# Kernel tuning notes

Hardware: AMD Instinct MI355X
Metric: run time of the kernel (lower is better)

Reference implementation:

```python
import jax, jax.numpy as jnp
import numpy as np

B = 65536       # batch size
C = 100         # num classes (len(cls_num_list))
ALPHA = 0.01    # soft-label blend weight
TAU = 2.0       # init arg tau
TEMP = 2.0      # distillation temperature
EPS = 1e-9


def _soft_ce(logits, soft_targets):
    # -(soft * log softmax(logits)).sum(1).mean()
    return -(soft_targets * jax.nn.log_softmax(logits, axis=1)).sum(axis=1).mean()


def _inverse_prior(prior):
    idx0 = jnp.argsort(prior)            # ascending sort permutation
    value = prior[idx0]                  # sorted values
    idx1 = jnp.argsort(idx0)             # rank of each element
    idx2 = prior.shape[0] - 1 - idx1     # mirrored rank
    return value[idx2]


def setup_inputs():
    key = jax.random.key(0)
    ks = jax.random.split(key, 8)
    cls_num = np.arange(500, 0, -5).astype(np.float32)  # matches init cls_num_list
    prior = jnp.asarray(cls_num / cls_num.sum(), dtype=jnp.float32)
    return {
        "output_logits": jax.random.normal(ks[0], (B, C), jnp.float32),
        "target": jax.random.randint(ks[1], (B,), 0, C),
        "cos_feature": jax.random.normal(ks[2], (C, C), jnp.float32),
        "old_pred": jax.random.normal(ks[3], (B, C), jnp.float32),
        "expert1_logits": jax.random.normal(ks[4], (B, C), jnp.float32),
        "expert2_logits": jax.random.normal(ks[5], (B, C), jnp.float32),
        "expert3_logits": jax.random.normal(ks[6], (B, C), jnp.float32),
        "output": jax.random.normal(ks[7], (B, C), jnp.float32),
        "prior": prior,
        "epoch": 5,
    }


def reference(output_logits, target, cos_feature, old_pred, expert1_logits,
              expert2_logits, expert3_logits, output, prior, epoch):
    num_classes = prior.shape[0]
    # ---- convert_to_soft_labels (vectorized: gather rows of sim matrix, softmax, blend) ----
    one_hot = jax.nn.one_hot(target, num_classes, dtype=jnp.float32)          # [B,C]
    sim_probs = jax.nn.softmax(cos_feature, axis=1)[target]                   # [B,C]
    label = (1.0 - ALPHA) * one_hot + ALPHA * sim_probs

    # ---- three expert soft cross-entropies ----
    log_prior = jnp.log(prior + EPS)
    loss = _soft_ce(expert1_logits, label)
    loss = loss + _soft_ce(expert2_logits + log_prior, label)
    inv_prior = _inverse_prior(prior)
    loss = loss + _soft_ce(expert3_logits + log_prior - TAU * jnp.log(inv_prior + EPS), label)

    # ---- bincount-normalized summed logits ----
    counts = jnp.bincount(target, length=num_classes).astype(jnp.float32)     # [C]
    num = counts[target][:, None]                                             # [B,1]
    expert_sum_logits = output / num                                          # [B,C]

    # ---- masked KL distillation (only rows where teacher argmax == target) ----
    teacher_index = jnp.argmax(old_pred, axis=1)                              # argmax(softmax)=argmax
    mask = (teacher_index == target).astype(jnp.float32)                      # [B]
    t = jax.nn.softmax(old_pred / TEMP, axis=1)                               # teacher probs
    s = jax.nn.log_softmax(expert_sum_logits / TEMP, axis=1)                  # student log-probs
    log_t = jnp.where(t > 0, jnp.log(t), 0.0)
    kl_per = (t * (log_t - s)).sum(axis=1)                                    # [B] per-row KL
    n_sel = mask.sum()
    kl_loss = jnp.where(n_sel > 0, (kl_per * mask).sum() / jnp.maximum(n_sel, 1.0), 0.0)
    kl_loss = kl_loss * (TEMP ** 2) * 3.0

    return loss, kl_loss, expert_sum_logits
```

## Files before the change

### kernel.cpp

```cpp
#include <hip/hip_runtime.h>
#include <math.h>

#define B_N 65536
#define C_N 100
constexpr float ALPHA = 0.01f;
constexpr float TAU   = 2.0f;
constexpr float TEMP  = 2.0f;
constexpr float EPSF  = 1e-9f;

template<int CTRL>
__device__ __forceinline__ float fadd_dpp(float x) {
    return x + __int_as_float(__builtin_amdgcn_update_dpp(
        0, __float_as_int(x), CTRL, 0xF, 0xF, true));
}
__device__ __forceinline__ float rowsum32(float x) {
    x = fadd_dpp<0xB1>(x);
    x = fadd_dpp<0x4E>(x);
    x = fadd_dpp<0x124>(x);
    x = fadd_dpp<0x128>(x);
    x = fadd_dpp<0x142>(x);
    return x;
}
template<int CTRL>
__device__ __forceinline__ void amax_dpp(unsigned &hi, unsigned &lo) {
    const unsigned yh = (unsigned)__builtin_amdgcn_update_dpp(0, (int)hi, CTRL, 0xF, 0xF, true);
    const unsigned yl = (unsigned)__builtin_amdgcn_update_dpp(0, (int)lo, CTRL, 0xF, 0xF, true);
    const bool take = (yh > hi) || (yh == hi && yl > lo);
    hi = take ? yh : hi;
    lo = take ? yl : lo;
}
__device__ __forceinline__ void rowamax32(unsigned &hi, unsigned &lo) {
    amax_dpp<0xB1>(hi, lo);
    amax_dpp<0x4E>(hi, lo);
    amax_dpp<0x124>(hi, lo);
    amax_dpp<0x128>(hi, lo);
    amax_dpp<0x142>(hi, lo);
}

__device__ __forceinline__ float wsum(float v) {
    #pragma unroll
    for (int o = 32; o; o >>= 1) v += __shfl_xor(v, o);
    return v;
}

__global__ void prep_k(const float* __restrict__ cosf, const float* __restrict__ prior,
                       const int* __restrict__ target,
                       float* __restrict__ sm, float* __restrict__ lp, float* __restrict__ c3,
                       int* __restrict__ counts) {
    const int b = blockIdx.x;
    if (b < 256) {
        __shared__ int h[C_N];
        for (int i = threadIdx.x; i < C_N; i += blockDim.x) h[i] = 0;
        __syncthreads();
        const int gid = b * blockDim.x + threadIdx.x;
        const int stride = 256 * blockDim.x;
        for (int i = gid; i < B_N; i += stride) atomicAdd(&h[target[i]], 1);
        __syncthreads();
        for (int i = threadIdx.x; i < C_N; i += blockDim.x)
            if (h[i]) atomicAdd(&counts[i], h[i]);
    } else if (b == 256) {
        __shared__ float sp[C_N];
        __shared__ float val[C_N];
        const int t = threadIdx.x;
        if (t < C_N) sp[t] = prior[t];
        __syncthreads();
        int rank = 0;
        float lpi = 0.f;
        if (t < C_N) {
            const float pi = sp[t];
            for (int j = 0; j < C_N; ++j) {
                const float pj = sp[j];
                rank += (pj < pi) || (pj == pi && j < t);
            }
            val[rank] = pi;
            lpi = __logf(pi + EPSF);
            lp[t] = lpi;
        }
        __syncthreads();
        if (t < C_N) {
            const float inv = val[C_N - 1 - rank];
            c3[t] = lpi - TAU * __logf(inv + EPSF);
        }
    } else {
        const int gw = (b - 257) * 4 + (threadIdx.x >> 6);
        const int lane = threadIdx.x & 63;
        for (int row = gw; row < C_N; row += 16) {
            const float* rp = cosf + row * C_N;
            const float v0 = rp[lane];
            const bool has1 = (lane + 64) < C_N;
            const float v1 = has1 ? rp[lane + 64] : -INFINITY;
            float m = fmaxf(v0, v1);
            #pragma unroll
            for (int o = 32; o; o >>= 1) m = fmaxf(m, __shfl_xor(m, o));
            const float e0 = __expf(v0 - m);
            const float e1 = has1 ? __expf(v1 - m) : 0.f;
            const float s = wsum(e0 + e1);
            const float is = 1.0f / s;
            sm[row * C_N + lane] = e0 * is;
            if (has1) sm[row * C_N + lane + 64] = e1 * is;
        }
    }
}

#define NBLK 2048
#define NWAVES (NBLK * 4)
#define PASSES (B_N / (2 * NWAVES))

__launch_bounds__(256)
__global__ void main_k(const int* __restrict__ target,
                       const float* __restrict__ e1p, const float* __restrict__ e2p,
                       const float* __restrict__ e3p, const float* __restrict__ opp,
                       const float* __restrict__ outp,
                       const float* __restrict__ sm, const float* __restrict__ lp,
                       const float* __restrict__ c3, const int* __restrict__ counts,
                       float* __restrict__ dout,
                       float* __restrict__ ploss, float* __restrict__ pkl, float* __restrict__ pn) {
    const int lane = threadIdx.x & 63;
    const int gl   = lane & 31;
    const int half = lane >> 5;
    const int wid  = (blockIdx.x * blockDim.x + threadIdx.x) >> 6;
    const bool act = gl < 25;
    const int c0 = 4 * gl;
    const bool own = (lane & 31) == 16;

    float4 LP = make_float4(0,0,0,0), CO = make_float4(0,0,0,0);
    if (act) {
        LP = *(const float4*)(lp + c0);
        CO = *(const float4*)(c3 + c0);
    }

    int tg[PASSES];
    #pragma unroll
    for (int r = 0; r < PASSES; ++r) tg[r] = target[2 * (wid + NWAVES * r) + half];
    float rnc[PASSES];
    #pragma unroll
    for (int r = 0; r < PASSES; ++r) rnc[r] = 1.0f / (float)counts[tg[r]];

    float lossA = 0.f, klA = 0.f, nA = 0.f;

    float4 E1, E2, E3, OP, OU, SM;
    E1 = E2 = E3 = OP = OU = SM = make_float4(0,0,0,0);
    {
        const int row0 = 2 * wid + half;
        const int base0 = row0 * C_N;
        if (act) {
            E1 = *(const float4*)(e1p + base0 + c0);
            E2 = *(const float4*)(e2p + base0 + c0);
            E3 = *(const float4*)(e3p + base0 + c0);
            OP = *(const float4*)(opp + base0 + c0);
            OU = *(const float4*)(outp + base0 + c0);
            SM = *(const float4*)(sm + tg[0] * C_N + c0);
        }
    }

    #pragma unroll
    for (int r = 0; r < PASSES; ++r) {
        const int row = 2 * (wid + NWAVES * r) + half;
        const int tgt = tg[r];
        const float rc = rnc[r];
        const int base = row * C_N;

        float4 nE1, nE2, nE3, nOP, nOU, nSM;
        nE1 = nE2 = nE3 = nOP = nOU = nSM = make_float4(0,0,0,0);
        if (r + 1 < PASSES) {
            const int nrow = 2 * (wid + NWAVES * (r + 1)) + half;
            const int nbase = nrow * C_N;
            if (act) {
                nE1 = *(const float4*)(e1p + nbase + c0);
                nE2 = *(const float4*)(e2p + nbase + c0);
                nE3 = *(const float4*)(e3p + nbase + c0);
                nOP = *(const float4*)(opp + nbase + c0);
                nOU = *(const float4*)(outp + nbase + c0);
                nSM = *(const float4*)(sm + tg[r + 1] * C_N + c0);
            }
        }

        const float la0 = (1.0f - ALPHA) * (c0     == tgt) + ALPHA * SM.x;
        const float la1 = (1.0f - ALPHA) * (c0 + 1 == tgt) + ALPHA * SM.y;
        const float la2 = (1.0f - ALPHA) * (c0 + 2 == tgt) + ALPHA * SM.z;
        const float la3 = (1.0f - ALPHA) * (c0 + 3 == tgt) + ALPHA * SM.w;

        const float l20 = E2.x + LP.x, l21 = E2.y + LP.y, l22 = E2.z + LP.z, l23 = E2.w + LP.w;
        const float l30 = E3.x + CO.x, l31 = E3.y + CO.y, l32 = E3.z + CO.z, l33 = E3.w + CO.w;

        float s1 = act ? (__expf(E1.x) + __expf(E1.y) + __expf(E1.z) + __expf(E1.w)) : 0.f;
        float s2 = act ? (__expf(l20) + __expf(l21) + __expf(l22) + __expf(l23)) : 0.f;
        float s3 = act ? (__expf(l30) + __expf(l31) + __expf(l32) + __expf(l33)) : 0.f;
        float dt = la0 * (E1.x + l20 + l30) + la1 * (E1.y + l21 + l31)
                 + la2 * (E1.z + l22 + l32) + la3 * (E1.w + l23 + l33);

        const float a0 = OP.x * 0.5f, a1 = OP.y * 0.5f, a2 = OP.z * 0.5f, a3 = OP.w * 0.5f;
        const float p0 = act ? __expf(a0) : 0.f;
        const float p1 = act ? __expf(a1) : 0.f;
        const float p2 = act ? __expf(a2) : 0.f;
        const float p3 = act ? __expf(a3) : 0.f;
        float zt = p0 + p1 + p2 + p3;

        float bv = OP.x; int bi = c0;
        if (OP.y > bv) { bv = OP.y; bi = c0 + 1; }
        if (OP.z > bv) { bv = OP.z; bi = c0 + 2; }
        if (OP.w > bv) { bv = OP.w; bi = c0 + 3; }
        unsigned bb = __float_as_uint(bv);
        bb = ((int)bb < 0) ? ~bb : (bb | 0x80000000u);
        unsigned khi = act ? bb : 0u;
        unsigned klo = act ? (unsigned)~bi : 0u;

        const float es0 = OU.x * rc, es1 = OU.y * rc, es2 = OU.z * rc, es3 = OU.w * rc;
        const float x0 = es0 * 0.5f, x1 = es1 * 0.5f, x2 = es2 * 0.5f, x3 = es3 * 0.5f;
        float zs = act ? (__expf(x0) + __expf(x1) + __expf(x2) + __expf(x3)) : 0.f;
        float D  = p0 * (a0 - x0) + p1 * (a1 - x1) + p2 * (a2 - x2) + p3 * (a3 - x3);

        s1 = rowsum32(s1);
        s2 = rowsum32(s2);
        s3 = rowsum32(s3);
        dt = rowsum32(dt);
        zt = rowsum32(zt);
        zs = rowsum32(zs);
        D  = rowsum32(D);
        rowamax32(khi, klo);

        const float ce  = __logf(s1 * s2 * s3) - dt;
        const int   mi  = (int)~klo;
        const float rzt = 1.0f / zt;
        const float kl  = D * rzt + __logf(zs * rzt);

        const bool sel = own && (mi == tgt);
        lossA += own ? ce : 0.f;
        klA   += sel ? kl : 0.f;
        nA    += sel ? 1.f : 0.f;

        if (act) {
            *(float2*)(dout + 2 + base + c0)     = make_float2(es0, es1);
            *(float2*)(dout + 2 + base + c0 + 2) = make_float2(es2, es3);
        }

        E1 = nE1; E2 = nE2; E3 = nE3; OP = nOP; OU = nOU; SM = nSM;
    }

    lossA = wsum(lossA);
    klA   = wsum(klA);
    nA    = wsum(nA);

    __shared__ float bl[4], bk[4], bn[4];
    const int wslot = threadIdx.x >> 6;
    if (lane == 0) { bl[wslot] = lossA; bk[wslot] = klA; bn[wslot] = nA; }
    __syncthreads();
    if (threadIdx.x == 0) {
        ploss[blockIdx.x] = bl[0] + bl[1] + bl[2] + bl[3];
        pkl[blockIdx.x]   = bk[0] + bk[1] + bk[2] + bk[3];
        pn[blockIdx.x]    = bn[0] + bn[1] + bn[2] + bn[3];
    }
}

__global__ void final_k(const float* __restrict__ ploss, const float* __restrict__ pkl,
                        const float* __restrict__ pn, float* __restrict__ dout) {
    __shared__ float sl[256], sk[256], sn[256];
    const int t = threadIdx.x;
    float l = 0.f, k = 0.f, n = 0.f;
    for (int i = t; i < NBLK; i += 256) { l += ploss[i]; k += pkl[i]; n += pn[i]; }
    sl[t] = l; sk[t] = k; sn[t] = n;
    __syncthreads();
    for (int s = 128; s; s >>= 1) {
        if (t < s) { sl[t] += sl[t + s]; sk[t] += sk[t + s]; sn[t] += sn[t + s]; }
        __syncthreads();
    }
    if (t == 0) {
        dout[0] = sl[0] / (float)B_N;
        const float kl = (sn[0] > 0.f) ? (sk[0] / fmaxf(sn[0], 1.f)) : 0.f;
        dout[1] = kl * (TEMP * TEMP) * 3.0f;
    }
}

extern "C" void kernel_launch(void* const* d_in, const int* in_sizes, int n_in,
                              void* d_out, int out_size, void* d_ws, size_t ws_size,
                              hipStream_t stream) {
    const int*   target = (const int*)  d_in[1];
    const float* cosf   = (const float*)d_in[2];
    const float* oldp   = (const float*)d_in[3];
    const float* e1     = (const float*)d_in[4];
    const float* e2     = (const float*)d_in[5];
    const float* e3     = (const float*)d_in[6];
    const float* outp   = (const float*)d_in[7];
    const float* prior  = (const float*)d_in[8];

    float* ws    = (float*)d_ws;
    float* sm    = ws;
    float* lp    = ws + 10000;
    float* c3    = ws + 10100;
    int*   cnts  = (int*)(ws + 10200);
    float* ploss = ws + 10304;
    float* pkl   = ploss + NBLK;
    float* pn    = pkl + NBLK;

    hipMemsetAsync(cnts, 0, C_N * sizeof(int), stream);
    prep_k<<<261, 256, 0, stream>>>(cosf, prior, target, sm, lp, c3, cnts);
    main_k<<<NBLK, 256, 0, stream>>>(target, e1, e2, e3, oldp, outp,
                                     sm, lp, c3, cnts, (float*)d_out, ploss, pkl, pn);
    final_k<<<1, 256, 0, stream>>>(ploss, pkl, pn, (float*)d_out);
}
```

Before: 53.15 us.

## Process one row pair per wave with 8192 blocks instead of multi-pass loop

```diff
diff --git a/kernel.cpp b/kernel.cpp
--- a/kernel.cpp
+++ b/kernel.cpp
@@ -7,6 +7,7 @@
 constexpr float TAU   = 2.0f;
 constexpr float TEMP  = 2.0f;
 constexpr float EPSF  = 1e-9f;
+constexpr float NEG_SENT = -1.0e30f;
 
 template<int CTRL>
 __device__ __forceinline__ float fadd_dpp(float x) {
@@ -102,9 +103,7 @@
     }
 }
 
-#define NBLK 2048
-#define NWAVES (NBLK * 4)
-#define PASSES (B_N / (2 * NWAVES))
+#define NBLK 8192
 
 __launch_bounds__(256)
 __global__ void main_k(const int* __restrict__ target,
@@ -118,132 +117,90 @@
     const int lane = threadIdx.x & 63;
     const int gl   = lane & 31;
     const int half = lane >> 5;
-    const int wid  = (blockIdx.x * blockDim.x + threadIdx.x) >> 6;
+    const int wslot = threadIdx.x >> 6;
+    const int gw   = blockIdx.x * 4 + wslot;
     const bool act = gl < 25;
     const int c0 = 4 * gl;
-    const bool own = (lane & 31) == 16;
+
+    const int row = 2 * gw + half;
+    const int tgt = target[row];
+    const float rc = 1.0f / (float)counts[tgt];
+    const int base = row * C_N;
 
     float4 LP = make_float4(0,0,0,0), CO = make_float4(0,0,0,0);
+    float4 E1, E2, E3, OP, OU, SM;
+    E1 = E2 = E3 = OP = OU = make_float4(NEG_SENT, NEG_SENT, NEG_SENT, NEG_SENT);
+    SM = make_float4(0,0,0,0);
     if (act) {
         LP = *(const float4*)(lp + c0);
         CO = *(const float4*)(c3 + c0);
-    }
-
-    int tg[PASSES];
-    #pragma unroll
-    for (int r = 0; r < PASSES; ++r) tg[r] = target[2 * (wid + NWAVES * r) + half];
-    float rnc[PASSES];
-    #pragma unroll
-    for (int r = 0; r < PASSES; ++r) rnc[r] = 1.0f / (float)counts[tg[r]];
-
-    float lossA = 0.f, klA = 0.f, nA = 0.f;
-
-    float4 E1, E2, E3, OP, OU, SM;
-    E1 = E2 = E3 = OP = OU = SM = make_float4(0,0,0,0);
-    {
-        const int row0 = 2 * wid + half;
-        const int base0 = row0 * C_N;
-        if (act) {
-            E1 = *(const float4*)(e1p + base0 + c0);
-            E2 = *(const float4*)(e2p + base0 + c0);
-            E3 = *(const float4*)(e3p + base0 + c0);
-            OP = *(const float4*)(opp + base0 + c0);
-            OU = *(const float4*)(outp + base0 + c0);
-            SM = *(const float4*)(sm + tg[0] * C_N + c0);
-        }
-    }
-
-    #pragma unroll
-    for (int r = 0; r < PASSES; ++r) {
-        const int row = 2 * (wid + NWAVES * r) + half;
-        const int tgt = tg[r];
-        const float rc = rnc[r];
-        const int base = row * C_N;
-
-        float4 nE1, nE2, nE3, nOP, nOU, nSM;
-        nE1 = nE2 = nE3 = nOP = nOU = nSM = make_float4(0,0,0,0);
-        if (r + 1 < PASSES) {
-            const int nrow = 2 * (wid + NWAVES * (r + 1)) + half;
-            const int nbase = nrow * C_N;
-            if (act) {
-                nE1 = *(const float4*)(e1p + nbase + c0);
-                nE2 = *(const float4*)(e2p + nbase + c0);
-                nE3 = *(const float4*)(e3p + nbase + c0);
-                nOP = *(const float4*)(opp + nbase + c0);
-                nOU = *(const float4*)(outp + nbase + c0);
-                nSM = *(const float4*)(sm + tg[r + 1] * C_N + c0);
-            }
-        }
-
-        const float la0 = (1.0f - ALPHA) * (c0     == tgt) + ALPHA * SM.x;
-        const float la1 = (1.0f - ALPHA) * (c0 + 1 == tgt) + ALPHA * SM.y;
-        const float la2 = (1.0f - ALPHA) * (c0 + 2 == tgt) + ALPHA * SM.z;
-        const float la3 = (1.0f - ALPHA) * (c0 + 3 == tgt) + ALPHA * SM.w;
-
-        const float l20 = E2.x + LP.x, l21 = E2.y + LP.y, l22 = E2.z + LP.z, l23 = E2.w + LP.w;
-        const float l30 = E3.x + CO.x, l31 = E3.y + CO.y, l32 = E3.z + CO.z, l33 = E3.w + CO.w;
-
-        float s1 = act ? (__expf(E1.x) + __expf(E1.y) + __expf(E1.z) + __expf(E1.w)) : 0.f;
-        float s2 = act ? (__expf(l20) + __expf(l21) + __expf(l22) + __expf(l23)) : 0.f;
-        float s3 = act ? (__expf(l30) + __expf(l31) + __expf(l32) + __expf(l33)) : 0.f;
-        float dt = la0 * (E1.x + l20 + l30) + la1 * (E1.y + l21 + l31)
-                 + la2 * (E1.z + l22 + l32) + la3 * (E1.w + l23 + l33);
-
-        const float a0 = OP.x * 0.5f, a1 = OP.y * 0.5f, a2 = OP.z * 0.5f, a3 = OP.w * 0.5f;
-        const float p0 = act ? __expf(a0) : 0.f;
-        const float p1 = act ? __expf(a1) : 0.f;
-        const float p2 = act ? __expf(a2) : 0.f;
-        const float p3 = act ? __expf(a3) : 0.f;
-        float zt = p0 + p1 + p2 + p3;
-
-        float bv = OP.x; int bi = c0;
-        if (OP.y > bv) { bv = OP.y; bi = c0 + 1; }
-        if (OP.z > bv) { bv = OP.z; bi = c0 + 2; }
-        if (OP.w > bv) { bv = OP.w; bi = c0 + 3; }
-        unsigned bb = __float_as_uint(bv);
-        bb = ((int)bb < 0) ? ~bb : (bb | 0x80000000u);
-        unsigned khi = act ? bb : 0u;
-        unsigned klo = act ? (unsigned)~bi : 0u;
-
-        const float es0 = OU.x * rc, es1 = OU.y * rc, es2 = OU.z * rc, es3 = OU.w * rc;
-        const float x0 = es0 * 0.5f, x1 = es1 * 0.5f, x2 = es2 * 0.5f, x3 = es3 * 0.5f;
-        float zs = act ? (__expf(x0) + __expf(x1) + __expf(x2) + __expf(x3)) : 0.f;
-        float D  = p0 * (a0 - x0) + p1 * (a1 - x1) + p2 * (a2 - x2) + p3 * (a3 - x3);
-
-        s1 = rowsum32(s1);
-        s2 = rowsum32(s2);
-        s3 = rowsum32(s3);
-        dt = rowsum32(dt);
-        zt = rowsum32(zt);
-        zs = rowsum32(zs);
-        D  = rowsum32(D);
-        rowamax32(khi, klo);
-
-        const float ce  = __logf(s1 * s2 * s3) - dt;
-        const int   mi  = (int)~klo;
-        const float rzt = 1.0f / zt;
-        const float kl  = D * rzt + __logf(zs * rzt);
-
-        const bool sel = own && (mi == tgt);
-        lossA += own ? ce : 0.f;
-        klA   += sel ? kl : 0.f;
-        nA    += sel ? 1.f : 0.f;
-
-        if (act) {
-            *(float2*)(dout + 2 + base + c0)     = make_float2(es0, es1);
-            *(float2*)(dout + 2 + base + c0 + 2) = make_float2(es2, es3);
-        }
-
-        E1 = nE1; E2 = nE2; E3 = nE3; OP = nOP; OU = nOU; SM = nSM;
-    }
-
-    lossA = wsum(lossA);
-    klA   = wsum(klA);
-    nA    = wsum(nA);
+        E1 = *(const float4*)(e1p + base + c0);
+        E2 = *(const float4*)(e2p + base + c0);
+        E3 = *(const float4*)(e3p + base + c0);
+        OP = *(const float4*)(opp + base + c0);
+        OU = *(const float4*)(outp + base + c0);
+        SM = *(const float4*)(sm + tgt * C_N + c0);
+    }
+
+    const float la0 = (1.0f - ALPHA) * (c0     == tgt) + ALPHA * SM.x;
+    const float la1 = (1.0f - ALPHA) * (c0 + 1 == tgt) + ALPHA * SM.y;
+    const float la2 = (1.0f - ALPHA) * (c0 + 2 == tgt) + ALPHA * SM.z;
+    const float la3 = (1.0f - ALPHA) * (c0 + 3 == tgt) + ALPHA * SM.w;
+
+    const float l20 = E2.x + LP.x, l21 = E2.y + LP.y, l22 = E2.z + LP.z, l23 = E2.w + LP.w;
+    const float l30 = E3.x + CO.x, l31 = E3.y + CO.y, l32 = E3.z + CO.z, l33 = E3.w + CO.w;
+
+    float s1 = __expf(E1.x) + __expf(E1.y) + __expf(E1.z) + __expf(E1.w);
+    float s2 = __expf(l20) + __expf(l21) + __expf(l22) + __expf(l23);
+    float s3 = __expf(l30) + __expf(l31) + __expf(l32) + __expf(l33);
+    float dt = la0 * (E1.x + l20 + l30) + la1 * (E1.y + l21 + l31)
+             + la2 * (E1.z + l22 + l32) + la3 * (E1.w + l23 + l33);
+
+    const float a0 = OP.x * 0.5f, a1 = OP.y * 0.5f, a2 = OP.z * 0.5f, a3 = OP.w * 0.5f;
+    const float p0 = __expf(a0), p1 = __expf(a1), p2 = __expf(a2), p3 = __expf(a3);
+    float zt = p0 + p1 + p2 + p3;
+
+    float bv = OP.x; int bi = c0;
+    if (OP.y > bv) { bv = OP.y; bi = c0 + 1; }
+    if (OP.z > bv) { bv = OP.z; bi = c0 + 2; }
+    if (OP.w > bv) { bv = OP.w; bi = c0 + 3; }
+    unsigned bb = __float_as_uint(bv);
+    bb = ((int)bb < 0) ? ~bb : (bb | 0x80000000u);
+    unsigned khi = bb, klo = (unsigned)~bi;
+
+    const float es0 = OU.x * rc, es1 = OU.y * rc, es2 = OU.z * rc, es3 = OU.w * rc;
+    const float x0 = es0 * 0.5f, x1 = es1 * 0.5f, x2 = es2 * 0.5f, x3 = es3 * 0.5f;
+    float zs = __expf(x0) + __expf(x1) + __expf(x2) + __expf(x3);
+    float D  = p0 * (a0 - x0) + p1 * (a1 - x1) + p2 * (a2 - x2) + p3 * (a3 - x3);
+
+    s1 = rowsum32(s1);
+    s2 = rowsum32(s2);
+    s3 = rowsum32(s3);
+    dt = rowsum32(dt);
+    zt = rowsum32(zt);
+    zs = rowsum32(zs);
+    D  = rowsum32(D);
+    rowamax32(khi, klo);
+
+    const float ce  = __logf(s1 * s2 * s3) - dt;
+    const int   mi  = (int)~klo;
+    const float rzt = 1.0f / zt;
+    const float kl  = D * rzt + __logf(zs * rzt);
+    const bool  sel = (mi == tgt);
+
+    if (act) {
+        *(float2*)(dout + 2 + base + c0)     = make_float2(es0, es1);
+        *(float2*)(dout + 2 + base + c0 + 2) = make_float2(es2, es3);
+    }
+
+    const float klm = sel ? kl : 0.f;
+    const float nm  = sel ? 1.f : 0.f;
+    const float lossW = __shfl(ce, 16) + __shfl(ce, 48);
+    const float klW   = __shfl(klm, 16) + __shfl(klm, 48);
+    const float nW    = __shfl(nm, 16) + __shfl(nm, 48);
 
     __shared__ float bl[4], bk[4], bn[4];
-    const int wslot = threadIdx.x >> 6;
-    if (lane == 0) { bl[wslot] = lossA; bk[wslot] = klA; bn[wslot] = nA; }
+    if (lane == 0) { bl[wslot] = lossW; bk[wslot] = klW; bn[wslot] = nW; }
     __syncthreads();
     if (threadIdx.x == 0) {
         ploss[blockIdx.x] = bl[0] + bl[1] + bl[2] + bl[3];
```

Measured after the change: 53.16 us. About the same (+0.0%).
